# Optimization experiments

Hardware: AMD Instinct MI355X
Metric: run time of the kernel (lower is better)

The kernel has to match this reference:

```python
import jax, jax.numpy as jnp
import numpy as np

B = 65536

def setup_inputs() -> dict:
    key = jax.random.key(0)
    ks = jax.random.split(key, 6)
    inp = {
        "x": jax.random.normal(ks[0], (B, 784), dtype=jnp.float32),
        "w_conv": jnp.ones((3, 3), dtype=jnp.float32),
        "w1": jax.random.normal(ks[1], (128, 676), dtype=jnp.float32) * 0.04,
        "b1": jnp.zeros((128,), dtype=jnp.float32),
        "w2": jax.random.normal(ks[2], (512, 128), dtype=jnp.float32) * 0.09,
        "b2": jnp.zeros((512,), dtype=jnp.float32),
        "w3": jax.random.normal(ks[3], (256, 512), dtype=jnp.float32) * 0.04,
        "b3": jnp.zeros((256,), dtype=jnp.float32),
        "w4": jax.random.normal(ks[4], (10, 256), dtype=jnp.float32) * 0.06,
        "b4": jnp.zeros((10,), dtype=jnp.float32),
    }
    return inp


def reference(x, w_conv, w1, b1, w2, b2, w3, b3, w4, b4):
    # x: [B, 784] -> [B, 1, 28, 28]; valid 3x3 conv -> [B, 1, 26, 26]
    img = x.reshape(-1, 1, 28, 28)
    kern = w_conv.reshape(1, 1, 3, 3)
    conv = jax.lax.conv_general_dilated(
        img, kern, window_strides=(1, 1), padding="VALID",
        dimension_numbers=("NCHW", "OIHW", "NCHW"))
    # Original detaches conv weights AND wraps output in torch.tensor(...),
    # which cuts the autograd graph at the conv output.
    h = jax.lax.stop_gradient(conv.reshape(conv.shape[0], -1))  # [B, 676]
    h = jax.nn.relu(h @ w1.T + b1)   # [B, 128]
    h = jax.nn.relu(h @ w2.T + b2)   # [B, 512]
    h = jax.nn.relu(h @ w3.T + b3)   # [B, 256]
    return h @ w4.T + b4             # [B, 10]
```

## Files before the change

kernel.cpp:

```cpp
#include <hip/hip_runtime.h>
#include <stdint.h>

typedef _Float16 half8 __attribute__((ext_vector_type(8)));
typedef float    f32x4 __attribute__((ext_vector_type(4)));

static __device__ __forceinline__ void async_cp16(const void* g, void* l) {
  __builtin_amdgcn_global_load_lds(
      (const __attribute__((address_space(1))) uint32_t*)g,
      (__attribute__((address_space(3))) uint32_t*)l,
      16, 0, 0);
}


static __device__ __forceinline__ void pack_one(
    const float* __restrict__ w, _Float16* __restrict__ dst, int idx,
    int N_src, int K, int NTC, int KSC, int KCH)
{
  const int e    = idx & 7;
  const int lane = (idx >> 3) & 63;
  int t = idx >> 9;
  const int nt_in = t % NTC; t /= NTC;
  const int ks_in = t % KSC; t /= KSC;
  const int kc    = t % KCH; t /= KCH;
  const int nc    = t;
  const int n = (nc * NTC + nt_in) * 16 + (lane & 15);
  const int k = (kc * KSC + ks_in) * 32 + ((lane >> 4) << 3) + e;
  const float val = (n < N_src) ? w[(size_t)n * K + k] : 0.0f;
  dst[idx] = (_Float16)val;
}

__global__ void pack_all(const float* __restrict__ w1, const float* __restrict__ wc,
                         const float* __restrict__ w2, const float* __restrict__ w3,
                         const float* __restrict__ w4,
                         _Float16* __restrict__ pw1, _Float16* __restrict__ pw2,
                         _Float16* __restrict__ pw3, _Float16* __restrict__ pw4)
{
  int idx = (int)blockIdx.x * 256 + (int)threadIdx.x;

  if (idx < 102400) {
    const int e    = idx & 7;
    const int lane = (idx >> 3) & 63;
    int t = idx >> 9;
    const int nt  = t & 7;
    const int ksg = t >> 3;
    const int n = nt * 16 + (lane & 15);
    const int k = ksg * 32 + ((lane >> 4) << 3) + e;
    float val = 0.0f;
    if (k < 784) {
      const int pr = k / 28, pc = k % 28;
      #pragma unroll
      for (int i = 0; i < 3; ++i) {
        #pragma unroll
        for (int j = 0; j < 3; ++j) {
          const int orow = pr - i, ocol = pc - j;
          if (orow >= 0 && orow < 26 && ocol >= 0 && ocol < 26)
            val += wc[i * 3 + j] * w1[n * 676 + orow * 26 + ocol];
        }
      }
    }
    pw1[idx] = (_Float16)val;
    return;
  }
  idx -= 102400;
  if (idx < 65536)  { pack_one(w2, pw2, idx, 512, 128, 8, 4, 1); return; }
  idx -= 65536;
  if (idx < 131072) { pack_one(w3, pw3, idx, 256, 512, 4, 8, 2); return; }
  idx -= 131072;
  if (idx < 4096)   { pack_one(w4, pw4, idx, 10, 256, 1, 8, 1); return; }
}


template<int KS_TOT, int KSC, int NT_TOT, int NTC, int KCH, int NC,
         bool A_FP32, bool RELU, bool OUT_F16, int N_REAL, int K_A>
__global__ __launch_bounds__(512)
void gemm_k(const void* __restrict__ Aptr, const _Float16* __restrict__ Bpk,
            const float* __restrict__ bias, void* __restrict__ Out)
{
  constexpr int CHUNK_BYTES = KSC * NTC * 64 * 16;
  constexpr int ROUNDS = CHUNK_BYTES / 8192;
  __shared__ char lds[CHUNK_BYTES];

  const int tid  = (int)threadIdx.x;
  const int lane = tid & 63;
  const int wid  = tid >> 6;
  const int ln   = lane & 15;
  const int hi   = lane >> 4;
  const int rowBase = (int)blockIdx.x * 128 + wid * 16;
  const int row0 = rowBase + hi * 4;

  auto loadA = [&](int ks) -> half8 {
    half8 h;
    if constexpr (A_FP32) {
      const int k0 = ks * 32 + hi * 8;
      if (k0 < K_A) {
        const float* ap = (const float*)Aptr + (size_t)(rowBase + ln) * K_A + k0;
        const f32x4 v0 = *(const f32x4*)ap;
        const f32x4 v1 = *(const f32x4*)(ap + 4);
        #pragma unroll
        for (int e = 0; e < 4; ++e) { h[e] = (_Float16)v0[e]; h[4 + e] = (_Float16)v1[e]; }
      } else {
        #pragma unroll
        for (int e = 0; e < 8; ++e) h[e] = (_Float16)0.0f;
      }
    } else {
      const _Float16* ap = (const _Float16*)Aptr + (size_t)(rowBase + ln) * K_A
                           + ks * 32 + hi * 8;
      h = *(const half8*)ap;
    }
    return h;
  };

  half8 afrag[(NC > 1) ? KS_TOT : 1];

  for (int nc = 0; nc < NC; ++nc) {
    f32x4 acc[NTC];
    #pragma unroll
    for (int nt = 0; nt < NTC; ++nt) {
      const int n_g = (nc * NTC + nt) * 16 + ln;
      const float bv = (n_g < N_REAL) ? bias[n_g] : 0.0f;
      f32x4 a = {bv, bv, bv, bv};
      acc[nt] = a;
    }

    #pragma unroll
    for (int kc = 0; kc < KCH; ++kc) {
      const char* csrc = (const char*)Bpk + (size_t)(nc * KCH + kc) * CHUNK_BYTES;
      #pragma unroll
      for (int r = 0; r < ROUNDS; ++r) {
        async_cp16(csrc + (size_t)(r * 8192 + tid * 16),
                   lds + r * 8192 + wid * 1024);
      }
      __syncthreads();

      #pragma unroll
      for (int ks = 0; ks < KSC; ++ks) {
        const int gks = kc * KSC + ks;
        half8 a;
        if constexpr (NC > 1) {
          if (nc == 0) { a = loadA(gks); afrag[gks] = a; }
          else         { a = afrag[gks]; }
        } else {
          a = loadA(gks);
        }
        #pragma unroll
        for (int nt = 0; nt < NTC; ++nt) {
          const half8 b = *(const half8*)(lds + ((size_t)(ks * NTC + nt) * 64 + lane) * 16);
          acc[nt] = __builtin_amdgcn_mfma_f32_16x16x32_f16(a, b, acc[nt], 0, 0, 0);
        }
      }
      __syncthreads();
    }

    #pragma unroll
    for (int nt = 0; nt < NTC; ++nt) {
      const int n_g = (nc * NTC + nt) * 16 + ln;
      #pragma unroll
      for (int r = 0; r < 4; ++r) {
        float v = acc[nt][r];
        if constexpr (RELU) v = v > 0.0f ? v : 0.0f;
        if constexpr (OUT_F16) {
          ((_Float16*)Out)[(size_t)(row0 + r) * (NT_TOT * 16) + n_g] = (_Float16)v;
        } else {
          if (n_g < N_REAL)
            ((float*)Out)[(size_t)(row0 + r) * N_REAL + n_g] = v;
        }
      }
    }
  }
}


extern "C" void kernel_launch(void* const* d_in, const int* in_sizes, int n_in,
                              void* d_out, int out_size, void* d_ws, size_t ws_size,
                              hipStream_t stream)
{
  const float* x     = (const float*)d_in[0];
  const float* wconv = (const float*)d_in[1];
  const float* w1    = (const float*)d_in[2];
  const float* b1    = (const float*)d_in[3];
  const float* w2    = (const float*)d_in[4];
  const float* b2    = (const float*)d_in[5];
  const float* w3    = (const float*)d_in[6];
  const float* b3    = (const float*)d_in[7];
  const float* w4    = (const float*)d_in[8];
  const float* b4    = (const float*)d_in[9];
  float* out = (float*)d_out;
  char*  ws  = (char*)d_ws;

  _Float16* pw1 = (_Float16*)(ws + 0);
  _Float16* pw2 = (_Float16*)(ws + 204800);
  _Float16* pw3 = (_Float16*)(ws + 335872);
  _Float16* pw4 = (_Float16*)(ws + 598016);
  _Float16* h1  = (_Float16*)(ws + 606208);
  _Float16* h2  = (_Float16*)(ws + 606208 + 16777216);
  _Float16* h3  = (_Float16*)(ws + 606208 + 16777216 + 67108864);

  pack_all<<<1184, 256, 0, stream>>>(w1, wconv, w2, w3, w4, pw1, pw2, pw3, pw4);

  gemm_k<25, 5,  8, 8, 5, 1, true,  true,  true, 128, 784>
      <<<512, 512, 0, stream>>>(x,  pw1, b1, h1);
  gemm_k< 4, 4, 32, 8, 1, 4, false, true,  true, 512, 128>
      <<<512, 512, 0, stream>>>(h1, pw2, b2, h2);
  gemm_k<16, 8, 16, 4, 2, 4, false, true,  true, 256, 512>
      <<<512, 512, 0, stream>>>(h2, pw3, b3, h3);
  gemm_k< 8, 8,  1, 1, 1, 1, false, false, false, 10, 256>
      <<<512, 512, 0, stream>>>(h3, pw4, b4, out);
}
```

Before: 368.9 us.

## Fuse four MLP GEMM layers into one kernel with LDS-resident activations

Replaces the four separate GEMM launches with one fused kernel. Each wave keeps its 16-row activation tile in a swizzled LDS scratch buffer between layers, so the fp16 intermediates h1/h2/h3 are never written to or read from global memory. Weight chunks are double-buffered in LDS with async global-to-LDS copies overlapping the MFMA work, and the layer-2 and layer-3 weights are interleaved so layer 3 accumulates over 128-wide slices of layer 2's output. The cost is high register pressure (24 accumulator fragments plus A fragments) under a 512x2 launch bound, and more LDS per block, which may limit occupancy or cause spills.

Result: faster. 340.8 us (-7.6%).

```diff
diff --git a/kernel.cpp b/kernel.cpp
--- a/kernel.cpp
+++ b/kernel.cpp
@@ -9,24 +9,6 @@
       (const __attribute__((address_space(1))) uint32_t*)g,
       (__attribute__((address_space(3))) uint32_t*)l,
       16, 0, 0);
-}
-
-
-static __device__ __forceinline__ void pack_one(
-    const float* __restrict__ w, _Float16* __restrict__ dst, int idx,
-    int N_src, int K, int NTC, int KSC, int KCH)
-{
-  const int e    = idx & 7;
-  const int lane = (idx >> 3) & 63;
-  int t = idx >> 9;
-  const int nt_in = t % NTC; t /= NTC;
-  const int ks_in = t % KSC; t /= KSC;
-  const int kc    = t % KCH; t /= KCH;
-  const int nc    = t;
-  const int n = (nc * NTC + nt_in) * 16 + (lane & 15);
-  const int k = (kc * KSC + ks_in) * 32 + ((lane >> 4) << 3) + e;
-  const float val = (n < N_src) ? w[(size_t)n * K + k] : 0.0f;
-  dst[idx] = (_Float16)val;
 }
 
 __global__ void pack_all(const float* __restrict__ w1, const float* __restrict__ wc,
@@ -37,48 +19,64 @@
 {
   int idx = (int)blockIdx.x * 256 + (int)threadIdx.x;
 
-  if (idx < 102400) {
-    const int e    = idx & 7;
-    const int lane = (idx >> 3) & 63;
-    int t = idx >> 9;
-    const int nt  = t & 7;
-    const int ksg = t >> 3;
+  if (idx < 114688) {
+    const int e = idx & 7, lane = (idx >> 3) & 63, f = idx >> 9;
+    const int nt = f & 7, gks = f >> 3;
     const int n = nt * 16 + (lane & 15);
-    const int k = ksg * 32 + ((lane >> 4) << 3) + e;
+    const int k = gks * 32 + ((lane >> 4) << 3) + e;
     float val = 0.0f;
     if (k < 784) {
       const int pr = k / 28, pc = k % 28;
       #pragma unroll
-      for (int i = 0; i < 3; ++i) {
+      for (int i = 0; i < 3; ++i)
         #pragma unroll
         for (int j = 0; j < 3; ++j) {
           const int orow = pr - i, ocol = pc - j;
           if (orow >= 0 && orow < 26 && ocol >= 0 && ocol < 26)
             val += wc[i * 3 + j] * w1[n * 676 + orow * 26 + ocol];
         }
-      }
     }
     pw1[idx] = (_Float16)val;
     return;
   }
-  idx -= 102400;
-  if (idx < 65536)  { pack_one(w2, pw2, idx, 512, 128, 8, 4, 1); return; }
+  idx -= 114688;
+  if (idx < 65536) {
+    const int e = idx & 7, lane = (idx >> 3) & 63, f = idx >> 9;
+    const int nt = f & 7, ks = (f >> 3) & 3, g = f >> 5;
+    const int n = g * 128 + nt * 16 + (lane & 15);
+    const int k = ks * 32 + ((lane >> 4) << 3) + e;
+    pw2[idx] = (_Float16)w2[n * 128 + k];
+    return;
+  }
   idx -= 65536;
-  if (idx < 131072) { pack_one(w3, pw3, idx, 256, 512, 4, 8, 2); return; }
+  if (idx < 131072) {
+    const int e = idx & 7, lane = (idx >> 3) & 63, f = idx >> 9;
+    const int nt = f & 7, ks = (f >> 3) & 3, c = f >> 5;
+    const int n = ((c & 1) * 8 + nt) * 16 + (lane & 15);
+    const int k = ((c >> 1) * 4 + ks) * 32 + ((lane >> 4) << 3) + e;
+    pw3[idx] = (_Float16)w3[n * 512 + k];
+    return;
+  }
   idx -= 131072;
-  if (idx < 4096)   { pack_one(w4, pw4, idx, 10, 256, 1, 8, 1); return; }
-}
-
-
-template<int KS_TOT, int KSC, int NT_TOT, int NTC, int KCH, int NC,
-         bool A_FP32, bool RELU, bool OUT_F16, int N_REAL, int K_A>
-__global__ __launch_bounds__(512)
-void gemm_k(const void* __restrict__ Aptr, const _Float16* __restrict__ Bpk,
-            const float* __restrict__ bias, void* __restrict__ Out)
+  if (idx < 4096) {
+    const int e = idx & 7, lane = (idx >> 3) & 63, f = idx >> 9;
+    const int n = lane & 15;
+    const int k = f * 32 + ((lane >> 4) << 3) + e;
+    pw4[idx] = (_Float16)((n < 10) ? w4[n * 256 + k] : 0.0f);
+    return;
+  }
+}
+
+__global__ __launch_bounds__(512, 2)
+void fused_mlp(const float* __restrict__ x,
+               const _Float16* __restrict__ pw1, const _Float16* __restrict__ pw2,
+               const _Float16* __restrict__ pw3, const _Float16* __restrict__ pw4,
+               const float* __restrict__ b1, const float* __restrict__ b2,
+               const float* __restrict__ b3, const float* __restrict__ b4,
+               float* __restrict__ out)
 {
-  constexpr int CHUNK_BYTES = KSC * NTC * 64 * 16;
-  constexpr int ROUNDS = CHUNK_BYTES / 8192;
-  __shared__ char lds[CHUNK_BYTES];
+  __shared__ char wbuf[2][32768];
+  __shared__ char tbuf[8][8192];
 
   const int tid  = (int)threadIdx.x;
   const int lane = tid & 63;
@@ -86,85 +84,169 @@
   const int ln   = lane & 15;
   const int hi   = lane >> 4;
   const int rowBase = (int)blockIdx.x * 128 + wid * 16;
-  const int row0 = rowBase + hi * 4;
-
-  auto loadA = [&](int ks) -> half8 {
+  char* tb = tbuf[wid];
+
+  auto stage = [&](int p) {
+    const char* src; int nb;
+    if (p < 7)       { src = (const char*)pw1 + (size_t)p * 32768; nb = 32768; }
+    else if (p < 19) {
+      const int j = p - 7, g = j / 3, r = j - g * 3;
+      if (r == 0)      src = (const char*)pw2 + (size_t)g * 32768;
+      else if (r == 1) src = (const char*)pw3 + (size_t)(2 * g) * 32768;
+      else             src = (const char*)pw3 + (size_t)(2 * g + 1) * 32768;
+      nb = 32768;
+    } else           { src = (const char*)pw4; nb = 8192; }
+    char* dst = wbuf[p & 1];
+    const int rounds = nb >> 13;
+    for (int r = 0; r < rounds; ++r)
+      async_cp16(src + r * 8192 + tid * 16, dst + r * 8192 + wid * 1024);
+  };
+
+  auto Bfrag = [&](const char* buf, int f) -> half8 {
+    return *(const half8*)(buf + (((f << 6) + lane) << 4));
+  };
+  auto twrite = [&](int row, int col, float v) {
+    const int off = (row << 9) + ((col << 1) ^ ((row & 7) << 4));
+    *(_Float16*)(tb + off) = (_Float16)v;
+  };
+  auto tread = [&](int ks) -> half8 {
+    const int off = (ln << 9) + (((ks << 6) + (hi << 4)) ^ ((ln & 7) << 4));
+    return *(const half8*)(tb + off);
+  };
+
+  const float* xrow = x + (size_t)(rowBase + ln) * 784;
+  auto loadA = [&](int gks) -> half8 {
     half8 h;
-    if constexpr (A_FP32) {
-      const int k0 = ks * 32 + hi * 8;
-      if (k0 < K_A) {
-        const float* ap = (const float*)Aptr + (size_t)(rowBase + ln) * K_A + k0;
-        const f32x4 v0 = *(const f32x4*)ap;
-        const f32x4 v1 = *(const f32x4*)(ap + 4);
-        #pragma unroll
-        for (int e = 0; e < 4; ++e) { h[e] = (_Float16)v0[e]; h[4 + e] = (_Float16)v1[e]; }
-      } else {
-        #pragma unroll
-        for (int e = 0; e < 8; ++e) h[e] = (_Float16)0.0f;
+    const int k0 = gks * 32 + hi * 8;
+    if (k0 < 784) {
+      const f32x4 v0 = *(const f32x4*)(xrow + k0);
+      const f32x4 v1 = *(const f32x4*)(xrow + k0 + 4);
+      #pragma unroll
+      for (int e = 0; e < 4; ++e) { h[e] = (_Float16)v0[e]; h[4 + e] = (_Float16)v1[e]; }
+    } else {
+      #pragma unroll
+      for (int e = 0; e < 8; ++e) h[e] = (_Float16)0.0f;
+    }
+    return h;
+  };
+
+  f32x4 acc1[8], acc3[16];
+  #pragma unroll
+  for (int nt = 0; nt < 8; ++nt) {
+    const float bv = b1[nt * 16 + ln];
+    f32x4 a = {bv, bv, bv, bv}; acc1[nt] = a;
+  }
+  #pragma unroll
+  for (int q = 0; q < 16; ++q) {
+    const float bv = b3[q * 16 + ln];
+    f32x4 a = {bv, bv, bv, bv}; acc3[q] = a;
+  }
+
+  stage(0);
+  __syncthreads();
+
+  #pragma unroll
+  for (int kc = 0; kc < 7; ++kc) {
+    stage(kc + 1);
+    const char* bw = wbuf[kc & 1];
+    half8 a[4];
+    #pragma unroll
+    for (int ks = 0; ks < 4; ++ks) a[ks] = loadA(kc * 4 + ks);
+    #pragma unroll
+    for (int ks = 0; ks < 4; ++ks)
+      #pragma unroll
+      for (int nt = 0; nt < 8; ++nt)
+        acc1[nt] = __builtin_amdgcn_mfma_f32_16x16x32_f16(
+            a[ks], Bfrag(bw, ks * 8 + nt), acc1[nt], 0, 0, 0);
+    __syncthreads();
+  }
+
+  half8 a1h[4];
+  #pragma unroll
+  for (int nt = 0; nt < 8; ++nt)
+    #pragma unroll
+    for (int r = 0; r < 4; ++r)
+      twrite(hi * 4 + r, nt * 16 + ln, fmaxf(acc1[nt][r], 0.0f));
+  #pragma unroll
+  for (int ks = 0; ks < 4; ++ks) a1h[ks] = tread(ks);
+
+  #pragma unroll
+  for (int g = 0; g < 4; ++g) {
+    const int p = 7 + 3 * g;
+    half8 a2c[4];
+
+    stage(p + 1);
+    {
+      const char* bw = wbuf[p & 1];
+      f32x4 acc2[8];
+      #pragma unroll
+      for (int nt = 0; nt < 8; ++nt) {
+        const float bv = b2[g * 128 + nt * 16 + ln];
+        f32x4 a = {bv, bv, bv, bv}; acc2[nt] = a;
       }
-    } else {
-      const _Float16* ap = (const _Float16*)Aptr + (size_t)(rowBase + ln) * K_A
-                           + ks * 32 + hi * 8;
-      h = *(const half8*)ap;
-    }
-    return h;
-  };
-
-  half8 afrag[(NC > 1) ? KS_TOT : 1];
-
-  for (int nc = 0; nc < NC; ++nc) {
-    f32x4 acc[NTC];
-    #pragma unroll
-    for (int nt = 0; nt < NTC; ++nt) {
-      const int n_g = (nc * NTC + nt) * 16 + ln;
-      const float bv = (n_g < N_REAL) ? bias[n_g] : 0.0f;
-      f32x4 a = {bv, bv, bv, bv};
-      acc[nt] = a;
-    }
-
-    #pragma unroll
-    for (int kc = 0; kc < KCH; ++kc) {
-      const char* csrc = (const char*)Bpk + (size_t)(nc * KCH + kc) * CHUNK_BYTES;
-      #pragma unroll
-      for (int r = 0; r < ROUNDS; ++r) {
-        async_cp16(csrc + (size_t)(r * 8192 + tid * 16),
-                   lds + r * 8192 + wid * 1024);
-      }
-      __syncthreads();
-
-      #pragma unroll
-      for (int ks = 0; ks < KSC; ++ks) {
-        const int gks = kc * KSC + ks;
-        half8 a;
-        if constexpr (NC > 1) {
-          if (nc == 0) { a = loadA(gks); afrag[gks] = a; }
-          else         { a = afrag[gks]; }
-        } else {
-          a = loadA(gks);
-        }
-        #pragma unroll
-        for (int nt = 0; nt < NTC; ++nt) {
-          const half8 b = *(const half8*)(lds + ((size_t)(ks * NTC + nt) * 64 + lane) * 16);
-          acc[nt] = __builtin_amdgcn_mfma_f32_16x16x32_f16(a, b, acc[nt], 0, 0, 0);
-        }
-      }
-      __syncthreads();
-    }
-
-    #pragma unroll
-    for (int nt = 0; nt < NTC; ++nt) {
-      const int n_g = (nc * NTC + nt) * 16 + ln;
-      #pragma unroll
-      for (int r = 0; r < 4; ++r) {
-        float v = acc[nt][r];
-        if constexpr (RELU) v = v > 0.0f ? v : 0.0f;
-        if constexpr (OUT_F16) {
-          ((_Float16*)Out)[(size_t)(row0 + r) * (NT_TOT * 16) + n_g] = (_Float16)v;
-        } else {
-          if (n_g < N_REAL)
-            ((float*)Out)[(size_t)(row0 + r) * N_REAL + n_g] = v;
-        }
-      }
+      #pragma unroll
+      for (int ks = 0; ks < 4; ++ks)
+        #pragma unroll
+        for (int nt = 0; nt < 8; ++nt)
+          acc2[nt] = __builtin_amdgcn_mfma_f32_16x16x32_f16(
+              a1h[ks], Bfrag(bw, ks * 8 + nt), acc2[nt], 0, 0, 0);
+      #pragma unroll
+      for (int nt = 0; nt < 8; ++nt)
+        #pragma unroll
+        for (int r = 0; r < 4; ++r)
+          twrite(hi * 4 + r, nt * 16 + ln, fmaxf(acc2[nt][r], 0.0f));
+      #pragma unroll
+      for (int ks = 0; ks < 4; ++ks) a2c[ks] = tread(ks);
+    }
+    __syncthreads();
+
+    stage(p + 2);
+    {
+      const char* bw = wbuf[(p + 1) & 1];
+      #pragma unroll
+      for (int ks = 0; ks < 4; ++ks)
+        #pragma unroll
+        for (int nt = 0; nt < 8; ++nt)
+          acc3[nt] = __builtin_amdgcn_mfma_f32_16x16x32_f16(
+              a2c[ks], Bfrag(bw, ks * 8 + nt), acc3[nt], 0, 0, 0);
+    }
+    __syncthreads();
+
+    stage(p + 3);
+    {
+      const char* bw = wbuf[p & 1];
+      #pragma unroll
+      for (int ks = 0; ks < 4; ++ks)
+        #pragma unroll
+        for (int nt = 0; nt < 8; ++nt)
+          acc3[8 + nt] = __builtin_amdgcn_mfma_f32_16x16x32_f16(
+              a2c[ks], Bfrag(bw, ks * 8 + nt), acc3[8 + nt], 0, 0, 0);
+    }
+    __syncthreads();
+  }
+
+  {
+    #pragma unroll
+    for (int q = 0; q < 16; ++q)
+      #pragma unroll
+      for (int r = 0; r < 4; ++r)
+        twrite(hi * 4 + r, q * 16 + ln, fmaxf(acc3[q][r], 0.0f));
+    half8 a3h[8];
+    #pragma unroll
+    for (int ks = 0; ks < 8; ++ks) a3h[ks] = tread(ks);
+
+    const float bv = (ln < 10) ? b4[ln] : 0.0f;
+    f32x4 acc4 = {bv, bv, bv, bv};
+    const char* bw = wbuf[1];
+    #pragma unroll
+    for (int ks = 0; ks < 8; ++ks)
+      acc4 = __builtin_amdgcn_mfma_f32_16x16x32_f16(
+          a3h[ks], Bfrag(bw, ks), acc4, 0, 0, 0);
+
+    if (ln < 10) {
+      #pragma unroll
+      for (int r = 0; r < 4; ++r)
+        out[(size_t)(rowBase + hi * 4 + r) * 10 + ln] = acc4[r];
     }
   }
 }
@@ -188,21 +270,10 @@
   char*  ws  = (char*)d_ws;
 
   _Float16* pw1 = (_Float16*)(ws + 0);
-  _Float16* pw2 = (_Float16*)(ws + 204800);
-  _Float16* pw3 = (_Float16*)(ws + 335872);
-  _Float16* pw4 = (_Float16*)(ws + 598016);
-  _Float16* h1  = (_Float16*)(ws + 606208);
-  _Float16* h2  = (_Float16*)(ws + 606208 + 16777216);
-  _Float16* h3  = (_Float16*)(ws + 606208 + 16777216 + 67108864);
-
-  pack_all<<<1184, 256, 0, stream>>>(w1, wconv, w2, w3, w4, pw1, pw2, pw3, pw4);
-
-  gemm_k<25, 5,  8, 8, 5, 1, true,  true,  true, 128, 784>
-      <<<512, 512, 0, stream>>>(x,  pw1, b1, h1);
-  gemm_k< 4, 4, 32, 8, 1, 4, false, true,  true, 512, 128>
-      <<<512, 512, 0, stream>>>(h1, pw2, b2, h2);
-  gemm_k<16, 8, 16, 4, 2, 4, false, true,  true, 256, 512>
-      <<<512, 512, 0, stream>>>(h2, pw3, b3, h3);
-  gemm_k< 8, 8,  1, 1, 1, 1, false, false, false, 10, 256>
-      <<<512, 512, 0, stream>>>(h3, pw4, b4, out);
-}
+  _Float16* pw2 = (_Float16*)(ws + 229376);
+  _Float16* pw3 = (_Float16*)(ws + 360448);
+  _Float16* pw4 = (_Float16*)(ws + 622592);
+
+  pack_all<<<1232, 256, 0, stream>>>(w1, wconv, w2, w3, w4, pw1, pw2, pw3, pw4);
+  fused_mlp<<<512, 512, 0, stream>>>(x, pw1, pw2, pw3, pw4, b1, b2, b3, b4, out);
+}
```
